# Kernel optimization log

Measured on AMD Instinct MI355X. Metric: run time of the kernel, lower is better.

The kernel has to match this reference:

```python
import jax, jax.numpy as jnp
import numpy as np

B, S, D, H, DFF = 4, 2048, 1024, 16, 4096
HD = D // H  # head_dim = 64


def rmsnorm(x, scale, eps=1e-6):
    var = jnp.mean(jnp.square(x), axis=-1, keepdims=True)
    return x * jax.lax.rsqrt(var + eps) * scale


def setup_inputs() -> dict:
    key = jax.random.key(0)
    ks = jax.random.split(key, 16)
    s = 1.0 / np.sqrt(D)
    inp = {
        "x": jax.random.normal(ks[0], (B, S, D), jnp.float32),
        "wq": jax.random.normal(ks[1], (D, D), jnp.float32) * s,
        "bq": jnp.zeros((D,), jnp.float32),
        "wk": jax.random.normal(ks[2], (D, D), jnp.float32) * s,
        "bk": jnp.zeros((D,), jnp.float32),
        "wv": jax.random.normal(ks[3], (D, D), jnp.float32) * s,
        "bv": jnp.zeros((D,), jnp.float32),
        "wbeta": jax.random.normal(ks[4], (D, H), jnp.float32) * s,
        "bbeta": jnp.zeros((H,), jnp.float32),
        "wo": jax.random.normal(ks[5], (D, D), jnp.float32) * s,
        "bo": jnp.zeros((D,), jnp.float32),
        "w1": jax.random.normal(ks[6], (D, DFF), jnp.float32) * s,
        "b1": jnp.zeros((DFF,), jnp.float32),
        "w2": jax.random.normal(ks[7], (DFF, D), jnp.float32) * (1.0 / np.sqrt(DFF)),
        "b2": jnp.zeros((D,), jnp.float32),
        "ln1_scale": jnp.ones((D,), jnp.float32),
        "ln2_scale": jnp.ones((D,), jnp.float32),
    }
    return inp


def gdn_attention(x, wq, bq, wk, bk, wv, bv, wbeta, bbeta, wo, bo):
    b, s, _ = x.shape
    q = (x @ wq + bq).reshape(b, s, H, HD)
    k = (x @ wk + bk).reshape(b, s, H, HD)
    v = (x @ wv + bv).reshape(b, s, H, HD)
    k = k / (jnp.linalg.norm(k, axis=-1, keepdims=True) + 1e-6)
    beta = jax.nn.sigmoid(x @ wbeta + bbeta)[..., None]  # (b, s, H, 1)

    # time-major for scan: (s, b, H, ...)
    q = jnp.transpose(q, (1, 0, 2, 3))
    k = jnp.transpose(k, (1, 0, 2, 3))
    v = jnp.transpose(v, (1, 0, 2, 3))
    beta = jnp.transpose(beta, (1, 0, 2, 3))

    def _step(Sm, inputs):
        q_t, k_t, v_t, beta_t = inputs
        Sk = jnp.einsum('bhde,bhe->bhd', Sm, k_t)
        delta = v_t - Sk
        Sm = Sm + beta_t[..., None] * jnp.einsum('bhd,bhe->bhde', delta, k_t)
        o_t = jnp.einsum('bhde,bhe->bhd', Sm, q_t)
        return Sm, o_t

    S0 = jnp.zeros((b, H, HD, HD), x.dtype)
    _, outputs = jax.lax.scan(_step, S0, (q, k, v, beta))
    outputs = jnp.transpose(outputs, (1, 0, 2, 3)).reshape(b, s, D)
    return outputs @ wo + bo


def reference(x, wq, bq, wk, bk, wv, bv, wbeta, bbeta, wo, bo,
              w1, b1, w2, b2, ln1_scale, ln2_scale):
    residual = x
    h = rmsnorm(x, ln1_scale)
    h = gdn_attention(h, wq, bq, wk, bk, wv, bv, wbeta, bbeta, wo, bo)
    x = h + residual
    residual = x
    h = rmsnorm(x, ln2_scale)
    h = jax.nn.gelu(h @ w1 + b1) @ w2 + b2
    return h + residual
```

## Files before the change

### kernel.cpp

```cpp
#include <hip/hip_runtime.h>

#define DEV __device__ __forceinline__

typedef short bf16x8 __attribute__((ext_vector_type(8)));
typedef float f32x4 __attribute__((ext_vector_type(4)));
typedef unsigned int uint;

#define SBAR()   asm volatile("s_barrier" ::: "memory")
#define WAITV(n) asm volatile("s_waitcnt vmcnt(" #n ")" ::: "memory")
#define WAITL()  asm volatile("s_waitcnt lgkmcnt(0)" ::: "memory")

DEV unsigned short f2b(float f) {
    uint u = __float_as_uint(f);
    u += 0x7fffu + ((u >> 16) & 1u);
    return (unsigned short)(u >> 16);
}
DEV uint packbf2(float a, float b) { return (uint)f2b(a) | ((uint)f2b(b) << 16); }
DEV float b2f(unsigned short s) { return __uint_as_float(((uint)s) << 16); }
DEV float b2f_lo(uint u) { return __uint_as_float(u << 16); }
DEV float b2f_hi(uint u) { return __uint_as_float(u & 0xffff0000u); }

DEV void async_cp16(const void* g, void* l) {
    __builtin_amdgcn_global_load_lds(
        (const __attribute__((address_space(1))) unsigned int*)g,
        (__attribute__((address_space(3))) unsigned int*)l, 16, 0, 0);
}

DEV float quad_sum(float x) {
    x += __int_as_float(__builtin_amdgcn_update_dpp(0, __float_as_int(x), 0xB1, 0xF, 0xF, true));
    x += __int_as_float(__builtin_amdgcn_update_dpp(0, __float_as_int(x), 0x4E, 0xF, 0xF, true));
    return x;
}

DEV float gelu_f(float u) {
    float p = u + 0.044715f * u * u * u;
    float e = __expf(-1.5957691216f * p);
    return __fdividef(u, 1.f + e);
}

DEV void dec8(uint4 p, float* o) {
    o[0] = b2f_lo(p.x); o[1] = b2f_hi(p.x); o[2] = b2f_lo(p.y); o[3] = b2f_hi(p.y);
    o[4] = b2f_lo(p.z); o[5] = b2f_hi(p.z); o[6] = b2f_lo(p.w); o[7] = b2f_hi(p.w);
}

__global__ __launch_bounds__(256) void transpose_cast_k(
    const float* __restrict__ in, unsigned short* __restrict__ out, int K, int N)
{
    __shared__ float tile[32][33];
    const int k0 = blockIdx.x * 32, n0 = blockIdx.y * 32;
    const int tx = threadIdx.x & 31, ty = threadIdx.x >> 5;
#pragma unroll
    for (int i = 0; i < 32; i += 8) {
        int n = n0 + tx;
        tile[ty + i][tx] = (n < N) ? in[(size_t)(k0 + ty + i) * N + n] : 0.0f;
    }
    __syncthreads();
#pragma unroll
    for (int i = 0; i < 32; i += 8) {
        out[(size_t)(n0 + ty + i) * K + (k0 + tx)] = f2b(tile[tx][ty + i]);
    }
}

__global__ void build_bias_k(const float* __restrict__ bq, const float* __restrict__ bk,
                             const float* __restrict__ bv, const float* __restrict__ bb,
                             float* __restrict__ outb)
{
    int i = blockIdx.x * 256 + threadIdx.x;
    if (i >= 3328) return;
    float v = 0.f;
    if (i < 1024)      v = bq[i];
    else if (i < 2048) v = bk[i - 1024];
    else if (i < 3072) v = bv[i - 2048];
    else if (i < 3088) v = bb[i - 3072];
    outb[i] = v;
}

__global__ __launch_bounds__(256) void rmsnorm_cast_k(
    const float* __restrict__ x, const float* __restrict__ scale,
    unsigned short* __restrict__ out)
{
    const int row = blockIdx.x;
    const int t = threadIdx.x;
    const float4 v = *(const float4*)(x + (size_t)row * 1024 + t * 4);
    float ss = v.x * v.x + v.y * v.y + v.z * v.z + v.w * v.w;
#pragma unroll
    for (int off = 1; off < 64; off <<= 1) ss += __shfl_xor(ss, off);
    __shared__ float wsum[4];
    if ((t & 63) == 0) wsum[t >> 6] = ss;
    __syncthreads();
    const float tot = wsum[0] + wsum[1] + wsum[2] + wsum[3];
    const float inv = rsqrtf(tot * (1.0f / 1024.0f) + 1e-6f);
    const float4 sc = *(const float4*)(scale + t * 4);
    uint lo = (uint)f2b(v.x * inv * sc.x) | ((uint)f2b(v.y * inv * sc.y) << 16);
    uint hi = (uint)f2b(v.z * inv * sc.z) | ((uint)f2b(v.w * inv * sc.w) << 16);
    uint2 pkd; pkd.x = lo; pkd.y = hi;
    *(uint2*)(out + (size_t)row * 1024 + t * 4) = pkd;
}

template <bool GELU, bool GUARD>
__global__ __launch_bounds__(512, 2) void gemm256(
    const unsigned short* __restrict__ A, const unsigned short* __restrict__ BT,
    const float* __restrict__ bias, unsigned short* __restrict__ C,
    int Nstride, int Nreal, int K)
{
    __shared__ __align__(16) unsigned short As[4][256 * 32];
    __shared__ __align__(16) unsigned short Bs[4][256 * 32];
    const int tid = threadIdx.x;
    const int wid = tid >> 6;
    const int lane = tid & 63;
    const int l16 = lane & 15, quad = lane >> 4;
    const int wm = wid & 1, wn = wid >> 1;
    const int m0 = blockIdx.x << 8, n0 = blockIdx.y << 8;

    const int srow = (wid << 5) + (lane >> 2);
    const int scol = ((lane & 3) ^ ((lane >> 3) & 3)) << 3;
    const unsigned short* Ag = A + (size_t)(m0 + srow) * K + scol;
    const unsigned short* Bg = BT + (size_t)(n0 + srow) * K + scol;
    const size_t rstep16 = (size_t)16 * K;
    const int ldst = wid << 10;

    f32x4 acc[8][4];
#pragma unroll
    for (int i = 0; i < 8; i++)
#pragma unroll
        for (int j = 0; j < 4; j++) acc[i][j] = (f32x4)0.f;

    const int ksw = (quad ^ ((l16 >> 1) & 3)) << 3;
    const int aoff = ((wm << 7) + l16) * 32 + ksw;
    const int boff = ((wn << 6) + l16) * 32 + ksw;

    const int nt = K >> 5;
    async_cp16(Ag, &As[0][ldst]);
    async_cp16(Ag + rstep16, &As[0][ldst + 512]);
    async_cp16(Bg, &Bs[0][ldst]);
    async_cp16(Bg + rstep16, &Bs[0][ldst + 512]);
    async_cp16(Ag + 32, &As[1][ldst]);
    async_cp16(Ag + 32 + rstep16, &As[1][ldst + 512]);
    async_cp16(Bg + 32, &Bs[1][ldst]);
    async_cp16(Bg + 32 + rstep16, &Bs[1][ldst + 512]);
    WAITV(4);
    SBAR();

    for (int tb = 0; tb < nt; tb += 4) {
#pragma unroll
        for (int u = 0; u < 4; ++u) {
            const int t = tb + u;
            const int pb = (u + 2) & 3;
            const bool st = (t + 2) < nt;
            const size_t kpre = (size_t)(t + 2) << 5;
            bf16x8 af[4], bfr[4];
#pragma unroll
            for (int mi = 0; mi < 4; mi++) af[mi] = *(const bf16x8*)&As[u][aoff + mi * 512];
#pragma unroll
            for (int ni = 0; ni < 4; ni++) bfr[ni] = *(const bf16x8*)&Bs[u][boff + ni * 512];
            if (st) {
                async_cp16(Ag + kpre, &As[pb][ldst]);
                async_cp16(Ag + kpre + rstep16, &As[pb][ldst + 512]);
            }
            SBAR();
            WAITL();
            __builtin_amdgcn_s_setprio(1);
#pragma unroll
            for (int mi = 0; mi < 4; mi++)
#pragma unroll
                for (int ni = 0; ni < 4; ni++)
                    acc[mi][ni] = __builtin_amdgcn_mfma_f32_16x16x32_bf16(af[mi], bfr[ni], acc[mi][ni], 0, 0, 0);
            __builtin_amdgcn_s_setprio(0);
            SBAR();
#pragma unroll
            for (int mi = 0; mi < 4; mi++) af[mi] = *(const bf16x8*)&As[u][aoff + (mi + 4) * 512];
            if (st) {
                async_cp16(Bg + kpre, &Bs[pb][ldst]);
                async_cp16(Bg + kpre + rstep16, &Bs[pb][ldst + 512]);
                WAITV(4);
            } else {
                WAITV(0);
            }
            SBAR();
            WAITL();
            __builtin_amdgcn_s_setprio(1);
#pragma unroll
            for (int mi = 0; mi < 4; mi++)
#pragma unroll
                for (int ni = 0; ni < 4; ni++)
                    acc[mi + 4][ni] = __builtin_amdgcn_mfma_f32_16x16x32_bf16(af[mi], bfr[ni], acc[mi + 4][ni], 0, 0, 0);
            __builtin_amdgcn_s_setprio(0);
            SBAR();
        }
    }

    float bv[4];
    const int ccol = n0 + (wn << 6) + l16;
#pragma unroll
    for (int ni = 0; ni < 4; ni++) bv[ni] = bias[ccol + ni * 16];
#pragma unroll
    for (int mi = 0; mi < 8; mi++) {
        const int row = m0 + (wm << 7) + mi * 16 + (quad << 2);
#pragma unroll
        for (int r = 0; r < 4; r++) {
            unsigned short* Crow = C + (size_t)(row + r) * Nstride + ccol;
#pragma unroll
            for (int ni = 0; ni < 4; ni++) {
                float v = acc[mi][ni][r] + bv[ni];
                if (GELU) v = gelu_f(v);
                if (!GUARD || (ccol + ni * 16) < Nreal) Crow[ni * 16] = f2b(v);
            }
        }
    }
}

template <bool ADD>
__global__ __launch_bounds__(512, 2) void gemm128n256(
    const unsigned short* __restrict__ A, const unsigned short* __restrict__ BT,
    const float* __restrict__ bias, const float* __restrict__ add,
    float* __restrict__ C, int N, int K)
{
    __shared__ __align__(16) unsigned short As[4][128 * 32];
    __shared__ __align__(16) unsigned short Bs[4][256 * 32];
    const int tid = threadIdx.x;
    const int wid = tid >> 6;
    const int lane = tid & 63;
    const int l16 = lane & 15, quad = lane >> 4;
    const int wm = wid & 1, wn = wid >> 1;
    const int m0 = blockIdx.x << 7, n0 = blockIdx.y << 8;

    const int arow = (wid << 4) + (lane >> 2);
    const int brow = (wid << 5) + (lane >> 2);
    const int scol = ((lane & 3) ^ ((lane >> 3) & 3)) << 3;
    const unsigned short* Ag = A + (size_t)(m0 + arow) * K + scol;
    const unsigned short* Bg = BT + (size_t)(n0 + brow) * K + scol;
    const size_t rstep16 = (size_t)16 * K;
    const int lda = wid << 9;
    const int ldb = wid << 10;

    f32x4 acc[4][4];
#pragma unroll
    for (int i = 0; i < 4; i++)
#pragma unroll
        for (int j = 0; j < 4; j++) acc[i][j] = (f32x4)0.f;

    const int ksw = (quad ^ ((l16 >> 1) & 3)) << 3;
    const int aoff = ((wm << 6) + l16) * 32 + ksw;
    const int boff = ((wn << 6) + l16) * 32 + ksw;

    const int nt = K >> 5;
    async_cp16(Ag, &As[0][lda]);
    async_cp16(Bg, &Bs[0][ldb]);
    async_cp16(Bg + rstep16, &Bs[0][ldb + 512]);
    async_cp16(Ag + 32, &As[1][lda]);
    async_cp16(Bg + 32, &Bs[1][ldb]);
    async_cp16(Bg + 32 + rstep16, &Bs[1][ldb + 512]);
    WAITV(3);
    SBAR();

    for (int tb = 0; tb < nt; tb += 4) {
#pragma unroll
        for (int u = 0; u < 4; ++u) {
            const int t = tb + u;
            const int pb = (u + 2) & 3;
            const bool st = (t + 2) < nt;
            const size_t kpre = (size_t)(t + 2) << 5;
            bf16x8 af[4], bfr[4];
#pragma unroll
            for (int mi = 0; mi < 4; mi++) af[mi] = *(const bf16x8*)&As[u][aoff + mi * 512];
#pragma unroll
            for (int ni = 0; ni < 4; ni++) bfr[ni] = *(const bf16x8*)&Bs[u][boff + ni * 512];
            if (st) {
                async_cp16(Ag + kpre, &As[pb][lda]);
                async_cp16(Bg + kpre, &Bs[pb][ldb]);
                async_cp16(Bg + kpre + rstep16, &Bs[pb][ldb + 512]);
            }
            SBAR();
            WAITL();
            __builtin_amdgcn_s_setprio(1);
#pragma unroll
            for (int mi = 0; mi < 4; mi++)
#pragma unroll
                for (int ni = 0; ni < 4; ni++)
                    acc[mi][ni] = __builtin_amdgcn_mfma_f32_16x16x32_bf16(af[mi], bfr[ni], acc[mi][ni], 0, 0, 0);
            __builtin_amdgcn_s_setprio(0);
            if (st) { WAITV(3); } else { WAITV(0); }
            SBAR();
        }
    }

    const int ccol = n0 + (wn << 6) + l16;
    float bv[4];
#pragma unroll
    for (int ni = 0; ni < 4; ni++) bv[ni] = bias[ccol + ni * 16];
#pragma unroll
    for (int mi = 0; mi < 4; mi++) {
        const int row = m0 + (wm << 6) + mi * 16 + (quad << 2);
#pragma unroll
        for (int r = 0; r < 4; r++) {
#pragma unroll
            for (int ni = 0; ni < 4; ni++) {
                size_t idx = (size_t)(row + r) * N + ccol + ni * 16;
                float v = acc[mi][ni][r] + bv[ni];
                if (ADD) v += add[idx];
                C[idx] = v;
            }
        }
    }
}


__global__ __launch_bounds__(256) void gdn_prep(
    unsigned short* __restrict__ qkv, unsigned short* __restrict__ Wg,
    unsigned short* __restrict__ ZTg, unsigned short* __restrict__ KTg)
{
    const int chunk = blockIdx.x, bh = blockIdx.y;
    const int b = bh >> 4, h = bh & 15;
    __shared__ float Ks[64 * 68];
    __shared__ float Ws[64 * 65];
    __shared__ float Zs[64 * 65];
    __shared__ float Asl[64 * 65];
    __shared__ float bs[64];
    const int tid = threadIdx.x;
    const int t = tid >> 2, c = tid & 3;
    unsigned short* rowp = qkv + (size_t)(b * 2048 + chunk * 64 + t) * 3200;

    float kn[16];
    {
        uint4 ka = *(const uint4*)(rowp + 1024 + h * 64 + 16 * c);
        uint4 kb = *(const uint4*)(rowp + 1024 + h * 64 + 16 * c + 8);
        dec8(ka, kn); dec8(kb, kn + 8);
    }
    float ss = 0.f;
#pragma unroll
    for (int j = 0; j < 16; j++) ss += kn[j] * kn[j];
    ss = quad_sum(ss);
    const float inv = 1.f / (sqrtf(ss) + 1e-6f);
#pragma unroll
    for (int j = 0; j < 16; j++) kn[j] *= inv;
#pragma unroll
    for (int j = 0; j < 16; j++) Ks[t * 68 + 16 * c + j] = kn[j];
    {
        uint4 p0, p1;
        p0.x = packbf2(kn[0], kn[1]);  p0.y = packbf2(kn[2], kn[3]);
        p0.z = packbf2(kn[4], kn[5]);  p0.w = packbf2(kn[6], kn[7]);
        p1.x = packbf2(kn[8], kn[9]);  p1.y = packbf2(kn[10], kn[11]);
        p1.z = packbf2(kn[12], kn[13]); p1.w = packbf2(kn[14], kn[15]);
        *(uint4*)(rowp + 1024 + h * 64 + 16 * c) = p0;
        *(uint4*)(rowp + 1024 + h * 64 + 16 * c + 8) = p1;
    }
    if (c == 0) bs[t] = 1.f / (1.f + __expf(-b2f(rowp[3072 + h])));
    __syncthreads();

    const float beta = bs[t];
#pragma unroll
    for (int j = 0; j < 16; j++) Ws[t * 65 + 16 * c + j] = beta * kn[j];
    {
        float vv[16];
        uint4 va = *(const uint4*)(rowp + 2048 + h * 64 + 16 * c);
        uint4 vb = *(const uint4*)(rowp + 2048 + h * 64 + 16 * c + 8);
        dec8(va, vv); dec8(vb, vv + 8);
#pragma unroll
        for (int j = 0; j < 16; j++) Zs[t * 65 + 16 * c + j] = beta * vv[j];
    }
    __syncthreads();

    {
        const int tt = tid >> 4, sx = tid & 15;
        float dm[4][4];
#pragma unroll
        for (int i = 0; i < 4; i++)
#pragma unroll
            for (int j = 0; j < 4; j++) dm[i][j] = 0.f;
        for (int d = 0; d < 64; d++) {
            float kt[4], ksv[4];
#pragma unroll
            for (int i = 0; i < 4; i++) kt[i] = Ks[(4 * tt + i) * 68 + d];
#pragma unroll
            for (int j = 0; j < 4; j++) ksv[j] = Ks[(4 * sx + j) * 68 + d];
#pragma unroll
            for (int i = 0; i < 4; i++)
#pragma unroll
                for (int j = 0; j < 4; j++) dm[i][j] += kt[i] * ksv[j];
        }
#pragma unroll
        for (int i = 0; i < 4; i++)
#pragma unroll
            for (int j = 0; j < 4; j++) {
                int T = 4 * tt + i, S_ = 4 * sx + j;
                Asl[T * 65 + S_] = (S_ < T) ? bs[T] * dm[i][j] : 0.f;
            }
    }
    __syncthreads();

    {
        const int wid = tid >> 6, lane = tid & 63;
        for (int qi = 0; qi < 4; qi++) {
            if (qi > 0) {
                const int tb = qi * 16 + wid * 4;
                float aw[4], az[4];
#pragma unroll
                for (int i = 0; i < 4; i++) { aw[i] = Ws[(tb + i) * 65 + lane]; az[i] = Zs[(tb + i) * 65 + lane]; }
                for (int s = 0; s < qi * 16; s++) {
                    float wsv = Ws[s * 65 + lane], zsv = Zs[s * 65 + lane];
#pragma unroll
                    for (int i = 0; i < 4; i++) {
                        float a = Asl[(tb + i) * 65 + s];
                        aw[i] -= a * wsv; az[i] -= a * zsv;
                    }
                }
#pragma unroll
                for (int i = 0; i < 4; i++) { Ws[(tb + i) * 65 + lane] = aw[i]; Zs[(tb + i) * 65 + lane] = az[i]; }
            }
            __syncthreads();
            if (wid == 0) {
                for (int T = qi * 16; T < qi * 16 + 16; T++) {
                    float a_ = Ws[T * 65 + lane];
                    for (int s = qi * 16; s < T; s++) a_ -= Asl[T * 65 + s] * Ws[s * 65 + lane];
                    Ws[T * 65 + lane] = a_;
                }
            } else if (wid == 1) {
                for (int T = qi * 16; T < qi * 16 + 16; T++) {
                    float a_ = Zs[T * 65 + lane];
                    for (int s = qi * 16; s < T; s++) a_ -= Asl[T * 65 + s] * Zs[s * 65 + lane];
                    Zs[T * 65 + lane] = a_;
                }
            }
            __syncthreads();
        }
    }

    const size_t cbase = ((size_t)bh * 32 + chunk) * 4096;
    {
#pragma unroll
        for (int half = 0; half < 2; half++) {
            uint4 w4;
            w4.x = packbf2(Ws[t * 65 + 16 * c + half * 8 + 0], Ws[t * 65 + 16 * c + half * 8 + 1]);
            w4.y = packbf2(Ws[t * 65 + 16 * c + half * 8 + 2], Ws[t * 65 + 16 * c + half * 8 + 3]);
            w4.z = packbf2(Ws[t * 65 + 16 * c + half * 8 + 4], Ws[t * 65 + 16 * c + half * 8 + 5]);
            w4.w = packbf2(Ws[t * 65 + 16 * c + half * 8 + 6], Ws[t * 65 + 16 * c + half * 8 + 7]);
            *(uint4*)(Wg + cbase + (size_t)((2 * c + half) * 64 + t) * 8) = w4;
        }
    }
    {
        const int jj = tid >> 2, tq = tid & 3;
#pragma unroll
        for (int half = 0; half < 2; half++) {
            uint4 z4;
            int i0 = half * 8;
            z4.x = packbf2(Zs[(16 * tq + i0 + 0) * 65 + jj], Zs[(16 * tq + i0 + 1) * 65 + jj]);
            z4.y = packbf2(Zs[(16 * tq + i0 + 2) * 65 + jj], Zs[(16 * tq + i0 + 3) * 65 + jj]);
            z4.z = packbf2(Zs[(16 * tq + i0 + 4) * 65 + jj], Zs[(16 * tq + i0 + 5) * 65 + jj]);
            z4.w = packbf2(Zs[(16 * tq + i0 + 6) * 65 + jj], Zs[(16 * tq + i0 + 7) * 65 + jj]);
            *(uint4*)(ZTg + cbase + (size_t)((2 * tq + half) * 64 + jj) * 8) = z4;
        }
    }
    {
        const int dd = tid >> 2, tq = tid & 3;
#pragma unroll
        for (int half = 0; half < 2; half++) {
            uint4 k4;
            int i0 = half * 8;
            k4.x = packbf2(Ks[(16 * tq + i0 + 0) * 68 + dd], Ks[(16 * tq + i0 + 1) * 68 + dd]);
            k4.y = packbf2(Ks[(16 * tq + i0 + 2) * 68 + dd], Ks[(16 * tq + i0 + 3) * 68 + dd]);
            k4.z = packbf2(Ks[(16 * tq + i0 + 4) * 68 + dd], Ks[(16 * tq + i0 + 5) * 68 + dd]);
            k4.w = packbf2(Ks[(16 * tq + i0 + 6) * 68 + dd], Ks[(16 * tq + i0 + 7) * 68 + dd]);
            *(uint4*)(KTg + cbase + (size_t)((2 * tq + half) * 64 + dd) * 8) = k4;
        }
    }
}

__global__ __launch_bounds__(256, 1) void gdn_prop_mfma(
    const unsigned short* __restrict__ Wg, const unsigned short* __restrict__ KTg,
    const unsigned short* __restrict__ ZTg, unsigned short* __restrict__ Sall,
    unsigned short* __restrict__ Yg)
{
    const int bh = blockIdx.x;
    __shared__ unsigned short WbU[4096];
    __shared__ unsigned short KTbU[4096];
    __shared__ unsigned short ZTbU[4096];
    __shared__ unsigned short SbU[4096];
    const int tid = threadIdx.x;
    const int wid = tid >> 6;
    const int lane = tid & 63;
    const int l16 = lane & 15, quad = lane >> 4;

    f32x4 Sacc[4];
#pragma unroll
    for (int dt = 0; dt < 4; dt++) Sacc[dt] = (f32x4)0.f;

    for (int ch = 0; ch < 32; ch++) {
        const size_t cbase = ((size_t)bh * 32 + ch) * 4096;
#pragma unroll
        for (int p = 0; p < 2; p++) {
            const int n = wid * 2 + p;
            async_cp16(Wg + cbase + n * 512 + lane * 8, &WbU[n * 512]);
            async_cp16(KTg + cbase + n * 512 + lane * 8, &KTbU[n * 512]);
            async_cp16(ZTg + cbase + n * 512 + lane * 8, &ZTbU[n * 512]);
        }
#pragma unroll
        for (int dt = 0; dt < 4; dt++) {
#pragma unroll
            for (int r = 0; r < 4; r++) {
                const int j = wid * 16 + quad * 4 + r;
                SbU[((2 * dt + (l16 >> 3)) * 64 + j) * 8 + (l16 & 7)] = f2b(Sacc[dt][r]);
            }
            const int d = dt * 16 + l16;
            uint2 sp;
            sp.x = packbf2(Sacc[dt][0], Sacc[dt][1]);
            sp.y = packbf2(Sacc[dt][2], Sacc[dt][3]);
            *(uint2*)(Sall + cbase + d * 64 + wid * 16 + quad * 4) = sp;
        }
        __syncthreads();

        f32x4 t1[4];
#pragma unroll
        for (int tt = 0; tt < 4; tt++) t1[tt] = (f32x4)0.f;
#pragma unroll
        for (int kh = 0; kh < 2; kh++) {
            const int g = kh * 4 + quad;
            bf16x8 afr = *(const bf16x8*)&SbU[(g * 64 + wid * 16 + l16) * 8];
#pragma unroll
            for (int tt = 0; tt < 4; tt++) {
                bf16x8 bfr = *(const bf16x8*)&WbU[(g * 64 + tt * 16 + l16) * 8];
                t1[tt] = __builtin_amdgcn_mfma_f32_16x16x32_bf16(afr, bfr, t1[tt], 0, 0, 0);
            }
        }
#pragma unroll
        for (int tt = 0; tt < 4; tt++) {
            const int t = tt * 16 + l16;
            const int gb = (t >> 3) * 64;
            unsigned short ybf[4];
#pragma unroll
            for (int r = 0; r < 4; r++) {
                const int j = wid * 16 + quad * 4 + r;
                const float z = b2f(ZTbU[(gb + j) * 8 + (t & 7)]);
                ybf[r] = f2b(z - t1[tt][r]);
            }
#pragma unroll
            for (int r = 0; r < 4; r++) {
                const int j = wid * 16 + quad * 4 + r;
                ZTbU[(gb + j) * 8 + (t & 7)] = ybf[r];
            }
            uint2 yp;
            yp.x = (uint)ybf[0] | ((uint)ybf[1] << 16);
            yp.y = (uint)ybf[2] | ((uint)ybf[3] << 16);
            *(uint2*)(Yg + cbase + t * 64 + wid * 16 + quad * 4) = yp;
        }
#pragma unroll
        for (int kh = 0; kh < 2; kh++) {
            const int g = kh * 4 + quad;
            bf16x8 afr = *(const bf16x8*)&ZTbU[(g * 64 + wid * 16 + l16) * 8];
#pragma unroll
            for (int dt = 0; dt < 4; dt++) {
                bf16x8 bfr = *(const bf16x8*)&KTbU[(g * 64 + dt * 16 + l16) * 8];
                Sacc[dt] = __builtin_amdgcn_mfma_f32_16x16x32_bf16(afr, bfr, Sacc[dt], 0, 0, 0);
            }
        }
        __syncthreads();
    }
}

__global__ __launch_bounds__(256) void gdn_out(
    const unsigned short* __restrict__ qkv, const unsigned short* __restrict__ Yg,
    const unsigned short* __restrict__ Sall, unsigned short* __restrict__ attn)
{
    const int chunk = blockIdx.x, bh = blockIdx.y;
    const int b = bh >> 4, h = bh & 15;
    __shared__ float Qf[64 * 68];
    __shared__ float SfT[64 * 68];
    __shared__ float Ms[64 * 65];
    __shared__ uint Kp[64 * 33];
    __shared__ uint Yp[64 * 34];
    const int tid = threadIdx.x;
    const int t = tid >> 2, c = tid & 3;
    const size_t cbase = ((size_t)bh * 32 + chunk) * 4096;

    {
        const unsigned short* rowp = qkv + (size_t)(b * 2048 + chunk * 64 + t) * 3200;
        float qv[16];
        uint4 qa = *(const uint4*)(rowp + h * 64 + 16 * c);
        uint4 qb = *(const uint4*)(rowp + h * 64 + 16 * c + 8);
        dec8(qa, qv); dec8(qb, qv + 8);
#pragma unroll
        for (int m = 0; m < 16; m++) Qf[t * 68 + 16 * c + m] = qv[m];
        uint4 ka = *(const uint4*)(rowp + 1024 + h * 64 + 16 * c);
        uint4 kb = *(const uint4*)(rowp + 1024 + h * 64 + 16 * c + 8);
        Kp[t * 33 + 8 * c + 0] = ka.x; Kp[t * 33 + 8 * c + 1] = ka.y;
        Kp[t * 33 + 8 * c + 2] = ka.z; Kp[t * 33 + 8 * c + 3] = ka.w;
        Kp[t * 33 + 8 * c + 4] = kb.x; Kp[t * 33 + 8 * c + 5] = kb.y;
        Kp[t * 33 + 8 * c + 6] = kb.z; Kp[t * 33 + 8 * c + 7] = kb.w;
        const unsigned short* yrow = Yg + cbase + t * 64 + 16 * c;
        uint4 ya = *(const uint4*)yrow;
        uint4 yb = *(const uint4*)(yrow + 8);
        Yp[t * 34 + 8 * c + 0] = ya.x; Yp[t * 34 + 8 * c + 1] = ya.y;
        Yp[t * 34 + 8 * c + 2] = ya.z; Yp[t * 34 + 8 * c + 3] = ya.w;
        Yp[t * 34 + 8 * c + 4] = yb.x; Yp[t * 34 + 8 * c + 5] = yb.y;
        Yp[t * 34 + 8 * c + 6] = yb.z; Yp[t * 34 + 8 * c + 7] = yb.w;
        const unsigned short* srow = Sall + cbase + t * 64 + 16 * c;
        float sv[16];
        uint4 sa = *(const uint4*)srow;
        uint4 sb = *(const uint4*)(srow + 8);
        dec8(sa, sv); dec8(sb, sv + 8);
#pragma unroll
        for (int m = 0; m < 16; m++) SfT[t * 68 + 16 * c + m] = sv[m];
    }
    __syncthreads();

    const int tt = tid >> 4, sx = tid & 15;
    {
        float dm[4][4];
#pragma unroll
        for (int i = 0; i < 4; i++)
#pragma unroll
            for (int j = 0; j < 4; j++) dm[i][j] = 0.f;
        for (int p = 0; p < 32; p++) {
            float q0[4], q1[4];
#pragma unroll
            for (int i = 0; i < 4; i++) {
                q0[i] = Qf[(4 * tt + i) * 68 + 2 * p];
                q1[i] = Qf[(4 * tt + i) * 68 + 2 * p + 1];
            }
#pragma unroll
            for (int j = 0; j < 4; j++) {
                uint kp = Kp[(4 * sx + j) * 33 + p];
                float kk0 = b2f_lo(kp), kk1 = b2f_hi(kp);
#pragma unroll
                for (int i = 0; i < 4; i++) dm[i][j] += q0[i] * kk0 + q1[i] * kk1;
            }
        }
#pragma unroll
        for (int i = 0; i < 4; i++)
#pragma unroll
            for (int j = 0; j < 4; j++) {
                int T = 4 * tt + i, S_ = 4 * sx + j;
                Ms[T * 65 + S_] = (S_ <= T) ? dm[i][j] : 0.f;
            }
    }
    __syncthreads();

    {
        float o[4][4];
#pragma unroll
        for (int i = 0; i < 4; i++)
#pragma unroll
            for (int j = 0; j < 4; j++) o[i][j] = 0.f;
        for (int d = 0; d < 64; d++) {
            float qv[4];
#pragma unroll
            for (int i = 0; i < 4; i++) qv[i] = Qf[(4 * tt + i) * 68 + d];
#pragma unroll
            for (int j = 0; j < 4; j++) {
                float sv = SfT[d * 68 + 4 * sx + j];
#pragma unroll
                for (int i = 0; i < 4; i++) o[i][j] += qv[i] * sv;
            }
        }
        for (int s = 0; s < 64; s++) {
            float mv[4];
#pragma unroll
            for (int i = 0; i < 4; i++) mv[i] = Ms[(4 * tt + i) * 65 + s];
            uint2 yp2 = *(const uint2*)&Yp[s * 34 + 2 * sx];
            float yv0 = b2f_lo(yp2.x), yv1 = b2f_hi(yp2.x), yv2 = b2f_lo(yp2.y), yv3 = b2f_hi(yp2.y);
#pragma unroll
            for (int i = 0; i < 4; i++) {
                o[i][0] += mv[i] * yv0; o[i][1] += mv[i] * yv1;
                o[i][2] += mv[i] * yv2; o[i][3] += mv[i] * yv3;
            }
        }
#pragma unroll
        for (int i = 0; i < 4; i++) {
            uint2 op; op.x = packbf2(o[i][0], o[i][1]); op.y = packbf2(o[i][2], o[i][3]);
            *(uint2*)(attn + (size_t)(b * 2048 + chunk * 64 + 4 * tt + i) * 1024 + h * 64 + 4 * sx) = op;
        }
    }
}

static constexpr size_t OFF_H     = 0;
static constexpr size_t OFF_WQKVT = OFF_H + 16777216;
static constexpr size_t OFF_WOT   = OFF_WQKVT + 6553600;
static constexpr size_t OFF_W1T   = OFF_WOT + 2097152;
static constexpr size_t OFF_W2T   = OFF_W1T + 8388608;
static constexpr size_t OFF_BIAS  = OFF_W2T + 8388608;
static constexpr size_t OFF_QKV   = OFF_BIAS + 16384;
static constexpr size_t OFF_ATTN  = OFF_QKV + 67108864;
static constexpr size_t OFF_Y1    = OFF_ATTN + 16777216;
static constexpr size_t OFF_WG    = OFF_Y1 + 33554432;
static constexpr size_t OFF_YG    = OFF_WG + 16777216;

extern "C" void kernel_launch(void* const* d_in, const int* in_sizes, int n_in,
                              void* d_out, int out_size, void* d_ws, size_t ws_size,
                              hipStream_t stream)
{
    const float* x     = (const float*)d_in[0];
    const float* wq    = (const float*)d_in[1];
    const float* bq    = (const float*)d_in[2];
    const float* wk    = (const float*)d_in[3];
    const float* bk    = (const float*)d_in[4];
    const float* wv    = (const float*)d_in[5];
    const float* bv    = (const float*)d_in[6];
    const float* wbeta = (const float*)d_in[7];
    const float* bbeta = (const float*)d_in[8];
    const float* wo    = (const float*)d_in[9];
    const float* bo    = (const float*)d_in[10];
    const float* w1    = (const float*)d_in[11];
    const float* b1    = (const float*)d_in[12];
    const float* w2    = (const float*)d_in[13];
    const float* b2    = (const float*)d_in[14];
    const float* ln1   = (const float*)d_in[15];
    const float* ln2   = (const float*)d_in[16];

    char* ws = (char*)d_ws;
    unsigned short* hbuf  = (unsigned short*)(ws + OFF_H);
    unsigned short* Sall  = (unsigned short*)(ws + OFF_H);
    unsigned short* wqkvT = (unsigned short*)(ws + OFF_WG);
    unsigned short* woT   = (unsigned short*)(ws + OFF_WOT);
    unsigned short* w1T   = (unsigned short*)(ws + OFF_W1T);
    unsigned short* w2T   = (unsigned short*)(ws + OFF_W2T);
    float*          biasc = (float*)(ws + OFF_BIAS);
    unsigned short* qkvU  = (unsigned short*)(ws + OFF_QKV);
    unsigned short* gbuf  = (unsigned short*)(ws + OFF_QKV);
    unsigned short* attn  = (unsigned short*)(ws + OFF_ATTN);
    float*          y1    = (float*)(ws + OFF_Y1);
    unsigned short* ZTg   = (unsigned short*)(ws + OFF_Y1);
    unsigned short* KTg   = (unsigned short*)(ws + OFF_Y1 + 16777216);
    unsigned short* Wg    = (unsigned short*)(ws + OFF_WG);
    unsigned short* Yg    = (unsigned short*)(ws + OFF_YG);
    float*          out   = (float*)d_out;

    transpose_cast_k<<<dim3(32, 32), 256, 0, stream>>>(wq, wqkvT,               1024, 1024);
    transpose_cast_k<<<dim3(32, 32), 256, 0, stream>>>(wk, wqkvT + 1024 * 1024, 1024, 1024);
    transpose_cast_k<<<dim3(32, 32), 256, 0, stream>>>(wv, wqkvT + 2048 * 1024, 1024, 1024);
    transpose_cast_k<<<dim3(32, 8),  256, 0, stream>>>(wbeta, wqkvT + 3072 * 1024, 1024, 16);
    transpose_cast_k<<<dim3(32, 32), 256, 0, stream>>>(wo, woT, 1024, 1024);
    transpose_cast_k<<<dim3(32, 128), 256, 0, stream>>>(w1, w1T, 1024, 4096);
    transpose_cast_k<<<dim3(128, 32), 256, 0, stream>>>(w2, w2T, 4096, 1024);
    build_bias_k<<<13, 256, 0, stream>>>(bq, bk, bv, bbeta, biasc);

    rmsnorm_cast_k<<<8192, 256, 0, stream>>>(x, ln1, hbuf);
    gemm256<false, true><<<dim3(32, 13), 512, 0, stream>>>(hbuf, wqkvT, biasc, qkvU, 3200, 3200, 1024);
    gdn_prep<<<dim3(32, 64), 256, 0, stream>>>(qkvU, Wg, ZTg, KTg);
    gdn_prop_mfma<<<64, 256, 0, stream>>>(Wg, KTg, ZTg, Sall, Yg);
    gdn_out<<<dim3(32, 64), 256, 0, stream>>>(qkvU, Yg, Sall, attn);
    gemm128n256<true><<<dim3(64, 4), 512, 0, stream>>>(attn, woT, bo, x, y1, 1024, 1024);
    rmsnorm_cast_k<<<8192, 256, 0, stream>>>(y1, ln2, hbuf);
    gemm256<true, false><<<dim3(32, 16), 512, 0, stream>>>(hbuf, w1T, b1, gbuf, 4096, 4096, 1024);
    gemm128n256<true><<<dim3(64, 4), 512, 0, stream>>>(gbuf, w2T, b2, y1, out, 1024, 4096);
}
```

Before: 653.9 us.

## Double-buffer MFMA fragments in registers to overlap LDS reads with compute

Both GEMM kernels now load the next k-tile's A/B fragments from LDS into a second register set while MFMAs run on the current set, ping-ponging between two fragment arrays. Each k-step now needs one barrier instead of two or four, and the explicit lgkmcnt waits are gone. The cost is more VGPRs (gemm256 holds 24 fragment vectors plus 128 accumulator registers' worth), which risks spills or lower occupancy under launch_bounds(512,2).

```diff
diff --git a/kernel.cpp b/kernel.cpp
--- a/kernel.cpp
+++ b/kernel.cpp
@@ -8,7 +8,6 @@
 
 #define SBAR()   asm volatile("s_barrier" ::: "memory")
 #define WAITV(n) asm volatile("s_waitcnt vmcnt(" #n ")" ::: "memory")
-#define WAITL()  asm volatile("s_waitcnt lgkmcnt(0)" ::: "memory")
 
 DEV unsigned short f2b(float f) {
     uint u = __float_as_uint(f);
@@ -97,6 +96,43 @@
     *(uint2*)(out + (size_t)row * 1024 + t * 4) = pkd;
 }
 
+#define G256_TILE(U, CA, CB, NA, NB)                                                        \
+    do {                                                                                    \
+        const int t_ = tb + (U);                                                            \
+        const bool st_ = (t_ + 2) < nt;                                                     \
+        if (st_) {                                                                          \
+            const size_t kp_ = (size_t)(t_ + 2) << 5;                                       \
+            async_cp16(Ag + kp_, &As[((U) + 2) & 3][ldst]);                                 \
+            async_cp16(Ag + kp_ + rstep16, &As[((U) + 2) & 3][ldst + 512]);                 \
+            async_cp16(Bg + kp_, &Bs[((U) + 2) & 3][ldst]);                                 \
+            async_cp16(Bg + kp_ + rstep16, &Bs[((U) + 2) & 3][ldst + 512]);                 \
+            WAITV(4);                                                                       \
+        } else {                                                                            \
+            WAITV(0);                                                                       \
+        }                                                                                   \
+        SBAR();                                                                             \
+        if ((t_ + 1) < nt) {                                                                \
+            _Pragma("unroll")                                                               \
+            for (int mi = 0; mi < 8; mi++) {                                                \
+                NA[mi] = *(const bf16x8*)&As[((U) + 1) & 3][aoff + mi * 512];               \
+            }                                                                               \
+            _Pragma("unroll")                                                               \
+            for (int ni = 0; ni < 4; ni++) {                                                \
+                NB[ni] = *(const bf16x8*)&Bs[((U) + 1) & 3][boff + ni * 512];               \
+            }                                                                               \
+        }                                                                                   \
+        __builtin_amdgcn_s_setprio(1);                                                      \
+        _Pragma("unroll")                                                                   \
+        for (int mi = 0; mi < 8; mi++) {                                                    \
+            _Pragma("unroll")                                                               \
+            for (int ni = 0; ni < 4; ni++) {                                                \
+                acc[mi][ni] = __builtin_amdgcn_mfma_f32_16x16x32_bf16(CA[mi], CB[ni],       \
+                                                                     acc[mi][ni], 0, 0, 0); \
+            }                                                                               \
+        }                                                                                   \
+        __builtin_amdgcn_s_setprio(0);                                                      \
+    } while (0)
+
 template <bool GELU, bool GUARD>
 __global__ __launch_bounds__(512, 2) void gemm256(
     const unsigned short* __restrict__ A, const unsigned short* __restrict__ BT,
@@ -140,53 +176,17 @@
     async_cp16(Bg + 32 + rstep16, &Bs[1][ldst + 512]);
     WAITV(4);
     SBAR();
+    bf16x8 fA0[8], fB0[4], fA1[8], fB1[4];
+#pragma unroll
+    for (int mi = 0; mi < 8; mi++) fA0[mi] = *(const bf16x8*)&As[0][aoff + mi * 512];
+#pragma unroll
+    for (int ni = 0; ni < 4; ni++) fB0[ni] = *(const bf16x8*)&Bs[0][boff + ni * 512];
 
     for (int tb = 0; tb < nt; tb += 4) {
-#pragma unroll
-        for (int u = 0; u < 4; ++u) {
-            const int t = tb + u;
-            const int pb = (u + 2) & 3;
-            const bool st = (t + 2) < nt;
-            const size_t kpre = (size_t)(t + 2) << 5;
-            bf16x8 af[4], bfr[4];
-#pragma unroll
-            for (int mi = 0; mi < 4; mi++) af[mi] = *(const bf16x8*)&As[u][aoff + mi * 512];
-#pragma unroll
-            for (int ni = 0; ni < 4; ni++) bfr[ni] = *(const bf16x8*)&Bs[u][boff + ni * 512];
-            if (st) {
-                async_cp16(Ag + kpre, &As[pb][ldst]);
-                async_cp16(Ag + kpre + rstep16, &As[pb][ldst + 512]);
-            }
-            SBAR();
-            WAITL();
-            __builtin_amdgcn_s_setprio(1);
-#pragma unroll
-            for (int mi = 0; mi < 4; mi++)
-#pragma unroll
-                for (int ni = 0; ni < 4; ni++)
-                    acc[mi][ni] = __builtin_amdgcn_mfma_f32_16x16x32_bf16(af[mi], bfr[ni], acc[mi][ni], 0, 0, 0);
-            __builtin_amdgcn_s_setprio(0);
-            SBAR();
-#pragma unroll
-            for (int mi = 0; mi < 4; mi++) af[mi] = *(const bf16x8*)&As[u][aoff + (mi + 4) * 512];
-            if (st) {
-                async_cp16(Bg + kpre, &Bs[pb][ldst]);
-                async_cp16(Bg + kpre + rstep16, &Bs[pb][ldst + 512]);
-                WAITV(4);
-            } else {
-                WAITV(0);
-            }
-            SBAR();
-            WAITL();
-            __builtin_amdgcn_s_setprio(1);
-#pragma unroll
-            for (int mi = 0; mi < 4; mi++)
-#pragma unroll
-                for (int ni = 0; ni < 4; ni++)
-                    acc[mi + 4][ni] = __builtin_amdgcn_mfma_f32_16x16x32_bf16(af[mi], bfr[ni], acc[mi + 4][ni], 0, 0, 0);
-            __builtin_amdgcn_s_setprio(0);
-            SBAR();
-        }
+        G256_TILE(0, fA0, fB0, fA1, fB1);
+        G256_TILE(1, fA1, fB1, fA0, fB0);
+        G256_TILE(2, fA0, fB0, fA1, fB1);
+        G256_TILE(3, fA1, fB1, fA0, fB0);
     }
 
     float bv[4];
@@ -208,6 +208,42 @@
         }
     }
 }
+
+#define G128_TILE(U, CA, CB, NA, NB)                                                        \
+    do {                                                                                    \
+        const int t_ = tb + (U);                                                            \
+        const bool st_ = (t_ + 2) < nt;                                                     \
+        if (st_) {                                                                          \
+            const size_t kp_ = (size_t)(t_ + 2) << 5;                                       \
+            async_cp16(Ag + kp_, &As[((U) + 2) & 3][lda]);                                  \
+            async_cp16(Bg + kp_, &Bs[((U) + 2) & 3][ldb]);                                  \
+            async_cp16(Bg + kp_ + rstep16, &Bs[((U) + 2) & 3][ldb + 512]);                  \
+            WAITV(3);                                                                       \
+        } else {                                                                            \
+            WAITV(0);                                                                       \
+        }                                                                                   \
+        SBAR();                                                                             \
+        if ((t_ + 1) < nt) {                                                                \
+            _Pragma("unroll")                                                               \
+            for (int mi = 0; mi < 4; mi++) {                                                \
+                NA[mi] = *(const bf16x8*)&As[((U) + 1) & 3][aoff + mi * 512];               \
+            }                                                                               \
+            _Pragma("unroll")                                                               \
+            for (int ni = 0; ni < 4; ni++) {                                                \
+                NB[ni] = *(const bf16x8*)&Bs[((U) + 1) & 3][boff + ni * 512];               \
+            }                                                                               \
+        }                                                                                   \
+        __builtin_amdgcn_s_setprio(1);                                                      \
+        _Pragma("unroll")                                                                   \
+        for (int mi = 0; mi < 4; mi++) {                                                    \
+            _Pragma("unroll")                                                               \
+            for (int ni = 0; ni < 4; ni++) {                                                \
+                acc[mi][ni] = __builtin_amdgcn_mfma_f32_16x16x32_bf16(CA[mi], CB[ni],       \
+                                                                     acc[mi][ni], 0, 0, 0); \
+            }                                                                               \
+        }                                                                                   \
+        __builtin_amdgcn_s_setprio(0);                                                      \
+    } while (0)
 
 template <bool ADD>
 __global__ __launch_bounds__(512, 2) void gemm128n256(
@@ -252,36 +288,17 @@
     async_cp16(Bg + 32 + rstep16, &Bs[1][ldb + 512]);
     WAITV(3);
     SBAR();
+    bf16x8 fA0[4], fB0[4], fA1[4], fB1[4];
+#pragma unroll
+    for (int mi = 0; mi < 4; mi++) fA0[mi] = *(const bf16x8*)&As[0][aoff + mi * 512];
+#pragma unroll
+    for (int ni = 0; ni < 4; ni++) fB0[ni] = *(const bf16x8*)&Bs[0][boff + ni * 512];
 
     for (int tb = 0; tb < nt; tb += 4) {
-#pragma unroll
-        for (int u = 0; u < 4; ++u) {
-            const int t = tb + u;
-            const int pb = (u + 2) & 3;
-            const bool st = (t + 2) < nt;
-            const size_t kpre = (size_t)(t + 2) << 5;
-            bf16x8 af[4], bfr[4];
-#pragma unroll
-            for (int mi = 0; mi < 4; mi++) af[mi] = *(const bf16x8*)&As[u][aoff + mi * 512];
-#pragma unroll
-            for (int ni = 0; ni < 4; ni++) bfr[ni] = *(const bf16x8*)&Bs[u][boff + ni * 512];
-            if (st) {
-                async_cp16(Ag + kpre, &As[pb][lda]);
-                async_cp16(Bg + kpre, &Bs[pb][ldb]);
-                async_cp16(Bg + kpre + rstep16, &Bs[pb][ldb + 512]);
-            }
-            SBAR();
-            WAITL();
-            __builtin_amdgcn_s_setprio(1);
-#pragma unroll
-            for (int mi = 0; mi < 4; mi++)
-#pragma unroll
-                for (int ni = 0; ni < 4; ni++)
-                    acc[mi][ni] = __builtin_amdgcn_mfma_f32_16x16x32_bf16(af[mi], bfr[ni], acc[mi][ni], 0, 0, 0);
-            __builtin_amdgcn_s_setprio(0);
-            if (st) { WAITV(3); } else { WAITV(0); }
-            SBAR();
-        }
+        G128_TILE(0, fA0, fB0, fA1, fB1);
+        G128_TILE(1, fA1, fB1, fA0, fB0);
+        G128_TILE(2, fA0, fB0, fA1, fB1);
+        G128_TILE(3, fA1, fB1, fA0, fB0);
     }
 
     const int ccol = n0 + (wn << 6) + l16;
```

Result: no change. 661.0 us (+1.1%).

## Port gdn_out to bf16 MFMA and emit S/Y in MFMA-ready layout

Applied to the files above, without the earlier changes.

The per-chunk output kernel now computes Q·K^T, Q·S and the masked M·Y products with bf16 MFMA instructions instead of scalar fp32 FMAs. To feed it, the propagation kernel writes S and Y chunks straight from its LDS fragment layout with wide 16-byte stores rather than strided 8-byte stores. The intra-chunk mask matrix is split into hi/lo bf16 parts so that precision stays close to fp32. This removes the scalar-ALU bottleneck in gdn_out, at the cost of bf16 rounding of Q and an extra LDS copy pass in the propagation loop.

```diff
diff --git a/kernel.cpp b/kernel.cpp
--- a/kernel.cpp
+++ b/kernel.cpp
@@ -467,8 +467,8 @@
 
 __global__ __launch_bounds__(256, 1) void gdn_prop_mfma(
     const unsigned short* __restrict__ Wg, const unsigned short* __restrict__ KTg,
-    const unsigned short* __restrict__ ZTg, unsigned short* __restrict__ Sall,
-    unsigned short* __restrict__ Yg)
+    const unsigned short* __restrict__ ZTg, unsigned short* __restrict__ Sg,
+    unsigned short* __restrict__ YTg)
 {
     const int bh = blockIdx.x;
     __shared__ unsigned short WbU[4096];
@@ -500,13 +500,15 @@
                 const int j = wid * 16 + quad * 4 + r;
                 SbU[((2 * dt + (l16 >> 3)) * 64 + j) * 8 + (l16 & 7)] = f2b(Sacc[dt][r]);
             }
-            const int d = dt * 16 + l16;
-            uint2 sp;
-            sp.x = packbf2(Sacc[dt][0], Sacc[dt][1]);
-            sp.y = packbf2(Sacc[dt][2], Sacc[dt][3]);
-            *(uint2*)(Sall + cbase + d * 64 + wid * 16 + quad * 4) = sp;
         }
         __syncthreads();
+
+        {
+            uint4 sa0 = *(const uint4*)&SbU[tid * 16];
+            uint4 sa1 = *(const uint4*)&SbU[tid * 16 + 8];
+            *(uint4*)(Sg + cbase + tid * 16) = sa0;
+            *(uint4*)(Sg + cbase + tid * 16 + 8) = sa1;
+        }
 
         f32x4 t1[4];
 #pragma unroll
@@ -537,10 +539,6 @@
                 const int j = wid * 16 + quad * 4 + r;
                 ZTbU[(gb + j) * 8 + (t & 7)] = ybf[r];
             }
-            uint2 yp;
-            yp.x = (uint)ybf[0] | ((uint)ybf[1] << 16);
-            yp.y = (uint)ybf[2] | ((uint)ybf[3] << 16);
-            *(uint2*)(Yg + cbase + t * 64 + wid * 16 + quad * 4) = yp;
         }
 #pragma unroll
         for (int kh = 0; kh < 2; kh++) {
@@ -552,121 +550,113 @@
                 Sacc[dt] = __builtin_amdgcn_mfma_f32_16x16x32_bf16(afr, bfr, Sacc[dt], 0, 0, 0);
             }
         }
+#pragma unroll
+        for (int pp = 0; pp < 2; pp++) {
+            const int p = lane * 2 + pp;
+            const int g = p >> 4, jj = p & 15;
+            const int off = (g * 64 + wid * 16 + jj) * 8;
+            uint4 yv = *(const uint4*)&ZTbU[off];
+            *(uint4*)(YTg + cbase + off) = yv;
+        }
         __syncthreads();
     }
 }
 
 __global__ __launch_bounds__(256) void gdn_out(
-    const unsigned short* __restrict__ qkv, const unsigned short* __restrict__ Yg,
-    const unsigned short* __restrict__ Sall, unsigned short* __restrict__ attn)
+    const unsigned short* __restrict__ qkv, const unsigned short* __restrict__ YTg,
+    const unsigned short* __restrict__ Sg, unsigned short* __restrict__ attn)
 {
     const int chunk = blockIdx.x, bh = blockIdx.y;
     const int b = bh >> 4, h = bh & 15;
-    __shared__ float Qf[64 * 68];
-    __shared__ float SfT[64 * 68];
-    __shared__ float Ms[64 * 65];
-    __shared__ uint Kp[64 * 33];
-    __shared__ uint Yp[64 * 34];
+    __shared__ unsigned short QbU[8 * 516];
+    __shared__ unsigned short KbU[8 * 516];
+    __shared__ unsigned short StU[8 * 516];
+    __shared__ unsigned short YtU[8 * 516];
+    __shared__ unsigned short MhU[8 * 516];
+    __shared__ unsigned short MlU[8 * 516];
     const int tid = threadIdx.x;
-    const int t = tid >> 2, c = tid & 3;
+    const int wid = tid >> 6, lane = tid & 63;
+    const int l16 = lane & 15, quad = lane >> 4;
     const size_t cbase = ((size_t)bh * 32 + chunk) * 4096;
 
     {
+        const int t = tid >> 2, c = tid & 3;
         const unsigned short* rowp = qkv + (size_t)(b * 2048 + chunk * 64 + t) * 3200;
-        float qv[16];
         uint4 qa = *(const uint4*)(rowp + h * 64 + 16 * c);
         uint4 qb = *(const uint4*)(rowp + h * 64 + 16 * c + 8);
-        dec8(qa, qv); dec8(qb, qv + 8);
-#pragma unroll
-        for (int m = 0; m < 16; m++) Qf[t * 68 + 16 * c + m] = qv[m];
         uint4 ka = *(const uint4*)(rowp + 1024 + h * 64 + 16 * c);
         uint4 kb = *(const uint4*)(rowp + 1024 + h * 64 + 16 * c + 8);
-        Kp[t * 33 + 8 * c + 0] = ka.x; Kp[t * 33 + 8 * c + 1] = ka.y;
-        Kp[t * 33 + 8 * c + 2] = ka.z; Kp[t * 33 + 8 * c + 3] = ka.w;
-        Kp[t * 33 + 8 * c + 4] = kb.x; Kp[t * 33 + 8 * c + 5] = kb.y;
-        Kp[t * 33 + 8 * c + 6] = kb.z; Kp[t * 33 + 8 * c + 7] = kb.w;
-        const unsigned short* yrow = Yg + cbase + t * 64 + 16 * c;
-        uint4 ya = *(const uint4*)yrow;
-        uint4 yb = *(const uint4*)(yrow + 8);
-        Yp[t * 34 + 8 * c + 0] = ya.x; Yp[t * 34 + 8 * c + 1] = ya.y;
-        Yp[t * 34 + 8 * c + 2] = ya.z; Yp[t * 34 + 8 * c + 3] = ya.w;
-        Yp[t * 34 + 8 * c + 4] = yb.x; Yp[t * 34 + 8 * c + 5] = yb.y;
-        Yp[t * 34 + 8 * c + 6] = yb.z; Yp[t * 34 + 8 * c + 7] = yb.w;
-        const unsigned short* srow = Sall + cbase + t * 64 + 16 * c;
-        float sv[16];
-        uint4 sa = *(const uint4*)srow;
-        uint4 sb = *(const uint4*)(srow + 8);
-        dec8(sa, sv); dec8(sb, sv + 8);
-#pragma unroll
-        for (int m = 0; m < 16; m++) SfT[t * 68 + 16 * c + m] = sv[m];
+        *(uint4*)&QbU[(2 * c) * 516 + t * 8]     = qa;
+        *(uint4*)&QbU[(2 * c + 1) * 516 + t * 8] = qb;
+        *(uint4*)&KbU[(2 * c) * 516 + t * 8]     = ka;
+        *(uint4*)&KbU[(2 * c + 1) * 516 + t * 8] = kb;
+        const int g = tid >> 5, row = (tid * 2) & 63;
+        uint4 s0 = *(const uint4*)(Sg + cbase + tid * 16);
+        uint4 s1 = *(const uint4*)(Sg + cbase + tid * 16 + 8);
+        *(uint4*)&StU[g * 516 + row * 8]       = s0;
+        *(uint4*)&StU[g * 516 + (row + 1) * 8] = s1;
+        uint4 y0 = *(const uint4*)(YTg + cbase + tid * 16);
+        uint4 y1 = *(const uint4*)(YTg + cbase + tid * 16 + 8);
+        *(uint4*)&YtU[g * 516 + row * 8]       = y0;
+        *(uint4*)&YtU[g * 516 + (row + 1) * 8] = y1;
     }
     __syncthreads();
 
-    const int tt = tid >> 4, sx = tid & 15;
-    {
-        float dm[4][4];
-#pragma unroll
-        for (int i = 0; i < 4; i++)
-#pragma unroll
-            for (int j = 0; j < 4; j++) dm[i][j] = 0.f;
-        for (int p = 0; p < 32; p++) {
-            float q0[4], q1[4];
-#pragma unroll
-            for (int i = 0; i < 4; i++) {
-                q0[i] = Qf[(4 * tt + i) * 68 + 2 * p];
-                q1[i] = Qf[(4 * tt + i) * 68 + 2 * p + 1];
-            }
-#pragma unroll
-            for (int j = 0; j < 4; j++) {
-                uint kp = Kp[(4 * sx + j) * 33 + p];
-                float kk0 = b2f_lo(kp), kk1 = b2f_hi(kp);
-#pragma unroll
-                for (int i = 0; i < 4; i++) dm[i][j] += q0[i] * kk0 + q1[i] * kk1;
-            }
-        }
-#pragma unroll
-        for (int i = 0; i < 4; i++)
-#pragma unroll
-            for (int j = 0; j < 4; j++) {
-                int T = 4 * tt + i, S_ = 4 * sx + j;
-                Ms[T * 65 + S_] = (S_ <= T) ? dm[i][j] : 0.f;
-            }
+    f32x4 m[4], o[4];
+#pragma unroll
+    for (int i = 0; i < 4; i++) { m[i] = (f32x4)0.f; o[i] = (f32x4)0.f; }
+
+#pragma unroll
+    for (int kh = 0; kh < 2; kh++) {
+        const int g = kh * 4 + quad;
+        bf16x8 afr = *(const bf16x8*)&QbU[g * 516 + (wid * 16 + l16) * 8];
+#pragma unroll
+        for (int st = 0; st < 4; st++) {
+            bf16x8 bk = *(const bf16x8*)&KbU[g * 516 + (st * 16 + l16) * 8];
+            m[st] = __builtin_amdgcn_mfma_f32_16x16x32_bf16(afr, bk, m[st], 0, 0, 0);
+        }
+#pragma unroll
+        for (int jt = 0; jt < 4; jt++) {
+            bf16x8 bs_ = *(const bf16x8*)&StU[g * 516 + (jt * 16 + l16) * 8];
+            o[jt] = __builtin_amdgcn_mfma_f32_16x16x32_bf16(afr, bs_, o[jt], 0, 0, 0);
+        }
+    }
+
+#pragma unroll
+    for (int st = 0; st < 4; st++) {
+#pragma unroll
+        for (int r = 0; r < 4; r++) {
+            const int t = wid * 16 + quad * 4 + r;
+            const int s = st * 16 + l16;
+            float v = (s <= t) ? m[st][r] : 0.f;
+            unsigned short hi = f2b(v);
+            unsigned short lo = f2b(v - b2f(hi));
+            const int addr = (s >> 3) * 516 + t * 8 + (s & 7);
+            MhU[addr] = hi;
+            MlU[addr] = lo;
+        }
     }
     __syncthreads();
 
-    {
-        float o[4][4];
-#pragma unroll
-        for (int i = 0; i < 4; i++)
-#pragma unroll
-            for (int j = 0; j < 4; j++) o[i][j] = 0.f;
-        for (int d = 0; d < 64; d++) {
-            float qv[4];
-#pragma unroll
-            for (int i = 0; i < 4; i++) qv[i] = Qf[(4 * tt + i) * 68 + d];
-#pragma unroll
-            for (int j = 0; j < 4; j++) {
-                float sv = SfT[d * 68 + 4 * sx + j];
-#pragma unroll
-                for (int i = 0; i < 4; i++) o[i][j] += qv[i] * sv;
-            }
-        }
-        for (int s = 0; s < 64; s++) {
-            float mv[4];
-#pragma unroll
-            for (int i = 0; i < 4; i++) mv[i] = Ms[(4 * tt + i) * 65 + s];
-            uint2 yp2 = *(const uint2*)&Yp[s * 34 + 2 * sx];
-            float yv0 = b2f_lo(yp2.x), yv1 = b2f_hi(yp2.x), yv2 = b2f_lo(yp2.y), yv3 = b2f_hi(yp2.y);
-#pragma unroll
-            for (int i = 0; i < 4; i++) {
-                o[i][0] += mv[i] * yv0; o[i][1] += mv[i] * yv1;
-                o[i][2] += mv[i] * yv2; o[i][3] += mv[i] * yv3;
-            }
-        }
-#pragma unroll
-        for (int i = 0; i < 4; i++) {
-            uint2 op; op.x = packbf2(o[i][0], o[i][1]); op.y = packbf2(o[i][2], o[i][3]);
-            *(uint2*)(attn + (size_t)(b * 2048 + chunk * 64 + 4 * tt + i) * 1024 + h * 64 + 4 * sx) = op;
+#pragma unroll
+    for (int kh = 0; kh < 2; kh++) {
+        const int g = kh * 4 + quad;
+        bf16x8 ah = *(const bf16x8*)&MhU[g * 516 + (wid * 16 + l16) * 8];
+        bf16x8 al = *(const bf16x8*)&MlU[g * 516 + (wid * 16 + l16) * 8];
+#pragma unroll
+        for (int jt = 0; jt < 4; jt++) {
+            bf16x8 by = *(const bf16x8*)&YtU[g * 516 + (jt * 16 + l16) * 8];
+            o[jt] = __builtin_amdgcn_mfma_f32_16x16x32_bf16(ah, by, o[jt], 0, 0, 0);
+            o[jt] = __builtin_amdgcn_mfma_f32_16x16x32_bf16(al, by, o[jt], 0, 0, 0);
+        }
+    }
+
+#pragma unroll
+    for (int jt = 0; jt < 4; jt++) {
+#pragma unroll
+        for (int r = 0; r < 4; r++) {
+            const int t = wid * 16 + quad * 4 + r;
+            attn[(size_t)(b * 2048 + chunk * 64 + t) * 1024 + h * 64 + jt * 16 + l16] = f2b(o[jt][r]);
         }
     }
 }
@@ -707,7 +697,7 @@
 
     char* ws = (char*)d_ws;
     unsigned short* hbuf  = (unsigned short*)(ws + OFF_H);
-    unsigned short* Sall  = (unsigned short*)(ws + OFF_H);
+    unsigned short* Sg    = (unsigned short*)(ws + OFF_H);
     unsigned short* wqkvT = (unsigned short*)(ws + OFF_WG);
     unsigned short* woT   = (unsigned short*)(ws + OFF_WOT);
     unsigned short* w1T   = (unsigned short*)(ws + OFF_W1T);
@@ -720,7 +710,7 @@
     unsigned short* ZTg   = (unsigned short*)(ws + OFF_Y1);
     unsigned short* KTg   = (unsigned short*)(ws + OFF_Y1 + 16777216);
     unsigned short* Wg    = (unsigned short*)(ws + OFF_WG);
-    unsigned short* Yg    = (unsigned short*)(ws + OFF_YG);
+    unsigned short* YTg   = (unsigned short*)(ws + OFF_YG);
     float*          out   = (float*)d_out;
 
     transpose_cast_k<<<dim3(32, 32), 256, 0, stream>>>(wq, wqkvT,               1024, 1024);
@@ -735,8 +725,8 @@
     rmsnorm_cast_k<<<8192, 256, 0, stream>>>(x, ln1, hbuf);
     gemm256<false, true><<<dim3(32, 13), 512, 0, stream>>>(hbuf, wqkvT, biasc, qkvU, 3200, 3200, 1024);
     gdn_prep<<<dim3(32, 64), 256, 0, stream>>>(qkvU, Wg, ZTg, KTg);
-    gdn_prop_mfma<<<64, 256, 0, stream>>>(Wg, KTg, ZTg, Sall, Yg);
-    gdn_out<<<dim3(32, 64), 256, 0, stream>>>(qkvU, Yg, Sall, attn);
+    gdn_prop_mfma<<<64, 256, 0, stream>>>(Wg, KTg, ZTg, Sg, YTg);
+    gdn_out<<<dim3(32, 64), 256, 0, stream>>>(qkvU, YTg, Sg, attn);
     gemm128n256<true><<<dim3(64, 4), 512, 0, stream>>>(attn, woT, bo, x, y1, 1024, 1024);
     rmsnorm_cast_k<<<8192, 256, 0, stream>>>(y1, ln2, hbuf);
     gemm256<true, false><<<dim3(32, 16), 512, 0, stream>>>(hbuf, w1T, b1, gbuf, 4096, 4096, 1024);
```

Result: faster. 626.7 us (-4.2%).
